# Optimization experiments

Hardware: AMD Instinct MI355X
Metric: run time of the kernel (lower is better)

The kernel has to match this reference:

```python
import jax, jax.numpy as jnp
import numpy as np

N, C, BINS = 4194304, 8, 10


def setup_inputs() -> dict:
    key = jax.random.key(0)
    k1, k2, k3 = jax.random.split(key, 3)
    pred = jax.random.normal(k1, (N, C), dtype=jnp.float32)
    target = jax.random.randint(k2, (N,), 0, C)
    # per-class loss weights (BaseLoss.reset_epoch output), strictly positive
    weight = jax.random.uniform(k3, (C,), dtype=jnp.float32) + 0.5
    return {"pred": pred, "target": target, "weight": weight, "bins": BINS}


def reference(pred, target, weight, bins):
    n_class = pred.shape[1]
    y = jax.nn.one_hot(target, n_class, dtype=pred.dtype)          # [N, C]
    # per-sample class weight broadcast to [N, C] (matches repeat in torch)
    w = jnp.broadcast_to(weight[target][:, None], pred.shape)      # [N, C]

    # gradient norm g = |sigmoid(pred) - y|, detached in the original
    g = jax.lax.stop_gradient(jnp.abs(jax.nn.sigmoid(pred) - y))   # [N, C]
    tot = pred.size

    # edges = arange(bins+1)/bins with edges[-1] += 1e-6, half-open bins:
    # bin index = floor(g * bins), clipped so g == 1.0 lands in the last bin.
    bin_idx = jnp.clip((g * bins).astype(jnp.int32), 0, bins - 1)  # [N, C]

    # single fused histogram pass (replaces the O(bins*N) masked loop)
    counts = jnp.zeros((bins,), pred.dtype).at[bin_idx.ravel()].add(1.0)
    n_nonempty = jnp.sum(counts > 0).astype(pred.dtype)
    per_bin_w = jnp.where(counts > 0, tot / jnp.maximum(counts, 1.0), 0.0)
    ghm_w = per_bin_w[bin_idx] / jnp.maximum(n_nonempty, 1.0)      # [N, C]
    ghm_w = jax.lax.stop_gradient(ghm_w)

    # binary_cross_entropy_with_logits, reduction='none':
    # softplus(x) - x*y  ==  max(x,0) - x*y + log1p(exp(-|x|))
    bce = jax.nn.softplus(pred) - pred * y                         # [N, C]

    return jnp.sum(w * bce * ghm_w) / jnp.sum(w)
```

## Files before the change

### kernel.cpp

```cpp
#include <hip/hip_runtime.h>


#define NROWS 4194304
#define BINS 10

constexpr int BLOCK = 256;
constexpr int MAXGRID = 2048;

__global__ __launch_bounds__(BLOCK) void ghm_main(
    const float* __restrict__ pred, const int* __restrict__ target,
    const float* __restrict__ weight, float* __restrict__ ws)
{
    __shared__ float wlds[8];
    const int tid = threadIdx.x;
    if (tid < 8) wlds[tid] = weight[tid];
    __syncthreads();

    float sP[10];
#pragma unroll
    for (int i = 0; i < 10; ++i) sP[i] = 0.f;
    unsigned cP[10];
#pragma unroll
    for (int i = 0; i < 10; ++i) cP[i] = 0u;
    float sumw = 0.f;

    const int stride = gridDim.x * BLOCK;

    constexpr float NLOG2E = -1.4426950408889634f;
    constexpr float LN2    = 0.6931471805599453f;
    constexpr float A0 = 2.1972245773362196f;
    constexpr float A1 = 1.3862943611198906f;
    constexpr float A2 = 0.8472978603872037f;
    constexpr float A3 = 0.4054651081081644f;
    const unsigned LUT0 = 0x1u, LUT1 = 0x41u, LUT2 = 0x1041u,
                   LUT3 = 0x41041u, LUT4 = 0x1041041u;

    for (int r = blockIdx.x * BLOCK + tid; r < NROWS; ) {
        unsigned aHi = 0u, aLo = 0u;
#pragma unroll
        for (int k = 0; k < 4; ++k, r += stride) {
            const float4 p0 = reinterpret_cast<const float4*>(pred)[2 * r];
            const float4 p1 = reinterpret_cast<const float4*>(pred)[2 * r + 1];
            const int t = target[r];
            const float w = wlds[t];
            sumw += w;
            const float wln2 = w * LN2;
            const float pv[8] = {p0.x, p0.y, p0.z, p0.w, p1.x, p1.y, p1.z, p1.w};
#pragma unroll
            for (int c = 0; c < 8; ++c) {
                const float p = pv[c];
                const float q = (c == t) ? -p : p;
                const float aq = __builtin_fabsf(q);
                const float e = __builtin_amdgcn_exp2f(aq * NLOG2E);
                const bool c0 = aq < A0, c1 = aq < A1, c2 = aq < A2, c3 = aq < A3;
                const bool qp = q >= 0.f;
                const float l = __builtin_amdgcn_logf(1.0f + e);
                const float v = fmaf(l, wln2, w * fmaxf(q, 0.f));
                const float vhi = qp ? v : 0.f;
                const float vlo = v - vhi;
                sP[0] += vhi;               sP[5] += vlo;
                sP[1] += c0 ? vhi : 0.f;    sP[6] += c0 ? vlo : 0.f;
                sP[2] += c1 ? vhi : 0.f;    sP[7] += c1 ? vlo : 0.f;
                sP[3] += c2 ? vhi : 0.f;    sP[8] += c2 ? vlo : 0.f;
                sP[4] += c3 ? vhi : 0.f;    sP[9] += c3 ? vlo : 0.f;
                unsigned lut = c0 ? LUT1 : LUT0;
                lut = c1 ? LUT2 : lut;
                lut = c2 ? LUT3 : lut;
                lut = c3 ? LUT4 : lut;
                const unsigned ih = qp ? lut : 0u;
                aHi += ih;
                aLo += lut - ih;
            }
        }
#pragma unroll
        for (int i = 0; i < 5; ++i) {
            cP[i]     += (aHi >> (6 * i)) & 63u;
            cP[5 + i] += (aLo >> (6 * i)) & 63u;
        }
    }

#pragma unroll
    for (int i = 0; i < 10; ++i) {
        float x = sP[i]; unsigned ci = cP[i];
#pragma unroll
        for (int o = 32; o >= 1; o >>= 1) {
            x  += __shfl_xor(x, o, 64);
            ci += __shfl_xor(ci, o, 64);
        }
        sP[i] = x; cP[i] = ci;
    }
    {
        float x = sumw;
#pragma unroll
        for (int o = 32; o >= 1; o >>= 1) x += __shfl_xor(x, o, 64);
        sumw = x;
    }

    __shared__ float red[4][21];
    const int lane = tid & 63, wv = tid >> 6;
    if (lane == 0) {
#pragma unroll
        for (int i = 0; i < 10; ++i) red[wv][i] = sP[i];
#pragma unroll
        for (int i = 0; i < 10; ++i) red[wv][10 + i] = (float)cP[i];
        red[wv][20] = sumw;
    }
    __syncthreads();
    if (tid < 21) {
        const float s = red[0][tid] + red[1][tid] + red[2][tid] + red[3][tid];
        const int slot = tid < 10 ? tid : (tid < 20 ? tid + 6 : 10);
        ws[blockIdx.x * 32 + slot] = s;
    }
}

__global__ __launch_bounds__(BLOCK) void ghm_final(
    const float* __restrict__ ws, float* __restrict__ out, int nblocks)
{
    float a21[21];
#pragma unroll
    for (int i = 0; i < 21; ++i) a21[i] = 0.f;

    for (int b = threadIdx.x; b < nblocks; b += BLOCK) {
#pragma unroll
        for (int i = 0; i < 10; ++i) a21[i] += ws[b * 32 + i];
#pragma unroll
        for (int i = 0; i < 10; ++i) a21[10 + i] += ws[b * 32 + 16 + i];
        a21[20] += ws[b * 32 + 10];
    }

#pragma unroll
    for (int i = 0; i < 21; ++i) {
        float x = a21[i];
#pragma unroll
        for (int o = 32; o >= 1; o >>= 1) x += __shfl_xor(x, o, 64);
        a21[i] = x;
    }

    __shared__ float red[4][21];
    const int tid = threadIdx.x;
    const int lane = tid & 63, wv = tid >> 6;
    if (lane == 0) {
#pragma unroll
        for (int i = 0; i < 21; ++i) red[wv][i] = a21[i];
    }
    __syncthreads();
    if (tid == 0) {
        float T[21];
#pragma unroll
        for (int i = 0; i < 21; ++i)
            T[i] = red[0][i] + red[1][i] + red[2][i] + red[3][i];
        float S[10], CN[10];
#pragma unroll
        for (int k = 0; k < 5; ++k) {
            const float shn = (k < 4) ? T[k + 1]      : 0.f;
            const float sln = (k < 4) ? T[5 + k + 1]  : 0.f;
            const float chn = (k < 4) ? T[10 + k + 1] : 0.f;
            const float cln = (k < 4) ? T[15 + k + 1] : 0.f;
            S[9 - k]  = T[k]      - shn;  CN[9 - k] = T[10 + k] - chn;
            S[k]      = T[5 + k]  - sln;  CN[k]     = T[15 + k] - cln;
        }
        int nne = 0; float acc = 0.f;
        const float tot = 33554432.0f;
#pragma unroll
        for (int i = 0; i < 10; ++i) {
            if (CN[i] > 0.5f) { nne++; acc += S[i] * (tot / CN[i]); }
        }
        out[0] = acc / (float)nne / (8.0f * T[20]);
    }
}

extern "C" void kernel_launch(void* const* d_in, const int* in_sizes, int n_in,
                              void* d_out, int out_size, void* d_ws, size_t ws_size,
                              hipStream_t stream) {
    const float* pred   = (const float*)d_in[0];
    const int*   target = (const int*)d_in[1];
    const float* weight = (const float*)d_in[2];
    float* out = (float*)d_out;

    int blocks = MAXGRID;
    if (ws_size < (size_t)MAXGRID * 128u) {
        const int cap = (int)(ws_size / 128u);
        blocks = 1;
        while (blocks * 2 <= cap && blocks * 2 < MAXGRID) blocks *= 2;
    }

    ghm_main<<<blocks, BLOCK, 0, stream>>>(pred, target, weight, (float*)d_ws);
    ghm_final<<<1, BLOCK, 0, stream>>>((const float*)d_ws, out, blocks);
}
```

Measured before the change: 56.00 us.

## Specialize main kernel for full grid with all loads issued up front

Adds a specialized kernel for the full 2048-block grid in which each thread handles exactly 8 rows. All target and pred loads are issued before any compute, which raises memory-level parallelism and drops the loop. The per-element math now uses 2-wide float vectors to encourage packed FP32 adds, and the kernel requests 3 blocks per CU via launch bounds. A general grid-stride fallback is kept for small workspaces; the cost is higher register pressure from holding 16 float4 values live at once.

```diff
diff --git a/kernel.cpp b/kernel.cpp
--- a/kernel.cpp
+++ b/kernel.cpp
@@ -5,9 +5,88 @@
 #define BINS 10
 
 constexpr int BLOCK = 256;
-constexpr int MAXGRID = 2048;
-
-__global__ __launch_bounds__(BLOCK) void ghm_main(
+constexpr int GRID  = 2048;
+constexpr int STRD  = GRID * BLOCK;
+
+typedef float f2 __attribute__((ext_vector_type(2)));
+
+__device__ __forceinline__ void elem8(
+    const float4 a, const float4 b, const int t, const float w,
+    f2& sp0, f2& sp1, f2& sp2, f2& sp3, f2& sp4,
+    unsigned& aAll, unsigned& aHi)
+{
+    constexpr float NLOG2E = -1.4426950408889634f;
+    constexpr float LN2    = 0.6931471805599453f;
+    constexpr float T0 = 2.1972245773362196f;
+    constexpr float T1 = 1.3862943611198906f;
+    constexpr float T2 = 0.8472978603872037f;
+    constexpr float T3 = 0.4054651081081644f;
+    const float wln2 = w * LN2;
+    const float pv[8] = {a.x, a.y, a.z, a.w, b.x, b.y, b.z, b.w};
+#pragma unroll
+    for (int c = 0; c < 8; ++c) {
+        const float p = pv[c];
+        const float q = (c == t) ? -p : p;
+        const float aq = __builtin_fabsf(q);
+        const float e = __builtin_amdgcn_exp2f(aq * NLOG2E);
+        const bool b0 = aq < T0, b1 = aq < T1, b2 = aq < T2, b3 = aq < T3;
+        const bool qp = q >= 0.f;
+        const float l = __builtin_amdgcn_logf(1.0f + e);
+        const float v = fmaf(l, wln2, w * fmaxf(q, 0.f));
+        f2 vp; vp.x = qp ? v : 0.f; vp.y = v - vp.x;
+        sp0 += vp;
+        f2 g;
+        g.x = b0 ? vp.x : 0.f; g.y = b0 ? vp.y : 0.f; sp1 += g;
+        g.x = b1 ? vp.x : 0.f; g.y = b1 ? vp.y : 0.f; sp2 += g;
+        g.x = b2 ? vp.x : 0.f; g.y = b2 ? vp.y : 0.f; sp3 += g;
+        g.x = b3 ? vp.x : 0.f; g.y = b3 ? vp.y : 0.f; sp4 += g;
+        unsigned lut = b0 ? 0x41u : 0x1u;
+        lut = b1 ? 0x1041u : lut;
+        lut = b2 ? 0x41041u : lut;
+        lut = b3 ? 0x1041041u : lut;
+        aAll += lut;
+        aHi  += qp ? lut : 0u;
+    }
+}
+
+__device__ __forceinline__ void block_reduce_store(
+    f2 sp0, f2 sp1, f2 sp2, f2 sp3, f2 sp4,
+    const unsigned* cA, const unsigned* cH, float sumw,
+    float* __restrict__ ws, int tid)
+{
+    float r21[21];
+    r21[0] = sp0.x; r21[1] = sp1.x; r21[2] = sp2.x; r21[3] = sp3.x; r21[4] = sp4.x;
+    r21[5] = sp0.y; r21[6] = sp1.y; r21[7] = sp2.y; r21[8] = sp3.y; r21[9] = sp4.y;
+#pragma unroll
+    for (int k = 0; k < 5; ++k) {
+        r21[10 + k] = (float)cH[k];
+        r21[15 + k] = (float)(cA[k] - cH[k]);
+    }
+    r21[20] = sumw;
+
+#pragma unroll
+    for (int i = 0; i < 21; ++i) {
+        float x = r21[i];
+#pragma unroll
+        for (int o = 32; o >= 1; o >>= 1) x += __shfl_xor(x, o, 64);
+        r21[i] = x;
+    }
+
+    __shared__ float red4[4][21];
+    const int lane = tid & 63, wv = tid >> 6;
+    if (lane == 0) {
+#pragma unroll
+        for (int i = 0; i < 21; ++i) red4[wv][i] = r21[i];
+    }
+    __syncthreads();
+    if (tid < 21) {
+        const float s = red4[0][tid] + red4[1][tid] + red4[2][tid] + red4[3][tid];
+        const int slot = tid < 10 ? tid : (tid < 20 ? tid + 6 : 10);
+        ws[blockIdx.x * 32 + slot] = s;
+    }
+}
+
+__global__ __launch_bounds__(BLOCK, 3) void ghm_main_s(
     const float* __restrict__ pred, const int* __restrict__ target,
     const float* __restrict__ weight, float* __restrict__ ws)
 {
@@ -16,101 +95,86 @@
     if (tid < 8) wlds[tid] = weight[tid];
     __syncthreads();
 
-    float sP[10];
-#pragma unroll
-    for (int i = 0; i < 10; ++i) sP[i] = 0.f;
-    unsigned cP[10];
-#pragma unroll
-    for (int i = 0; i < 10; ++i) cP[i] = 0u;
+    const int r0 = blockIdx.x * BLOCK + tid;
+    const float4* __restrict__ p4 = reinterpret_cast<const float4*>(pred);
+
+    int tt[8];
+#pragma unroll
+    for (int i = 0; i < 8; ++i) tt[i] = target[r0 + i * STRD];
+
+    float4 c0a = p4[2 * (size_t)(r0 + 0 * STRD)], c0b = p4[2 * (size_t)(r0 + 0 * STRD) + 1];
+    float4 c1a = p4[2 * (size_t)(r0 + 1 * STRD)], c1b = p4[2 * (size_t)(r0 + 1 * STRD) + 1];
+    float4 c2a = p4[2 * (size_t)(r0 + 2 * STRD)], c2b = p4[2 * (size_t)(r0 + 2 * STRD) + 1];
+    float4 c3a = p4[2 * (size_t)(r0 + 3 * STRD)], c3b = p4[2 * (size_t)(r0 + 3 * STRD) + 1];
+
+    float wr[8];
+#pragma unroll
+    for (int i = 0; i < 8; ++i) wr[i] = wlds[tt[i]];
+
+    float4 n0a = p4[2 * (size_t)(r0 + 4 * STRD)], n0b = p4[2 * (size_t)(r0 + 4 * STRD) + 1];
+    float4 n1a = p4[2 * (size_t)(r0 + 5 * STRD)], n1b = p4[2 * (size_t)(r0 + 5 * STRD) + 1];
+    float4 n2a = p4[2 * (size_t)(r0 + 6 * STRD)], n2b = p4[2 * (size_t)(r0 + 6 * STRD) + 1];
+    float4 n3a = p4[2 * (size_t)(r0 + 7 * STRD)], n3b = p4[2 * (size_t)(r0 + 7 * STRD) + 1];
+
+    f2 sp0 = {0, 0}, sp1 = {0, 0}, sp2 = {0, 0}, sp3 = {0, 0}, sp4 = {0, 0};
+    unsigned cA[5] = {0, 0, 0, 0, 0}, cH[5] = {0, 0, 0, 0, 0};
+    unsigned aAll = 0u, aHi = 0u;
+    const float sumw = ((wr[0] + wr[1]) + (wr[2] + wr[3])) +
+                       ((wr[4] + wr[5]) + (wr[6] + wr[7]));
+
+    elem8(c0a, c0b, tt[0], wr[0], sp0, sp1, sp2, sp3, sp4, aAll, aHi);
+    elem8(c1a, c1b, tt[1], wr[1], sp0, sp1, sp2, sp3, sp4, aAll, aHi);
+    elem8(c2a, c2b, tt[2], wr[2], sp0, sp1, sp2, sp3, sp4, aAll, aHi);
+    elem8(c3a, c3b, tt[3], wr[3], sp0, sp1, sp2, sp3, sp4, aAll, aHi);
+#pragma unroll
+    for (int k = 0; k < 5; ++k) {
+        cA[k] += (aAll >> (6 * k)) & 63u;
+        cH[k] += (aHi  >> (6 * k)) & 63u;
+    }
+    aAll = 0u; aHi = 0u;
+
+    elem8(n0a, n0b, tt[4], wr[4], sp0, sp1, sp2, sp3, sp4, aAll, aHi);
+    elem8(n1a, n1b, tt[5], wr[5], sp0, sp1, sp2, sp3, sp4, aAll, aHi);
+    elem8(n2a, n2b, tt[6], wr[6], sp0, sp1, sp2, sp3, sp4, aAll, aHi);
+    elem8(n3a, n3b, tt[7], wr[7], sp0, sp1, sp2, sp3, sp4, aAll, aHi);
+#pragma unroll
+    for (int k = 0; k < 5; ++k) {
+        cA[k] += (aAll >> (6 * k)) & 63u;
+        cH[k] += (aHi  >> (6 * k)) & 63u;
+    }
+
+    block_reduce_store(sp0, sp1, sp2, sp3, sp4, cA, cH, sumw, ws, tid);
+}
+
+__global__ __launch_bounds__(BLOCK) void ghm_main_d(
+    const float* __restrict__ pred, const int* __restrict__ target,
+    const float* __restrict__ weight, float* __restrict__ ws)
+{
+    __shared__ float wlds[8];
+    const int tid = threadIdx.x;
+    if (tid < 8) wlds[tid] = weight[tid];
+    __syncthreads();
+
+    f2 sp0 = {0, 0}, sp1 = {0, 0}, sp2 = {0, 0}, sp3 = {0, 0}, sp4 = {0, 0};
+    unsigned cA[5] = {0, 0, 0, 0, 0}, cH[5] = {0, 0, 0, 0, 0};
     float sumw = 0.f;
-
     const int stride = gridDim.x * BLOCK;
-
-    constexpr float NLOG2E = -1.4426950408889634f;
-    constexpr float LN2    = 0.6931471805599453f;
-    constexpr float A0 = 2.1972245773362196f;
-    constexpr float A1 = 1.3862943611198906f;
-    constexpr float A2 = 0.8472978603872037f;
-    constexpr float A3 = 0.4054651081081644f;
-    const unsigned LUT0 = 0x1u, LUT1 = 0x41u, LUT2 = 0x1041u,
-                   LUT3 = 0x41041u, LUT4 = 0x1041041u;
-
-    for (int r = blockIdx.x * BLOCK + tid; r < NROWS; ) {
-        unsigned aHi = 0u, aLo = 0u;
-#pragma unroll
-        for (int k = 0; k < 4; ++k, r += stride) {
-            const float4 p0 = reinterpret_cast<const float4*>(pred)[2 * r];
-            const float4 p1 = reinterpret_cast<const float4*>(pred)[2 * r + 1];
-            const int t = target[r];
-            const float w = wlds[t];
-            sumw += w;
-            const float wln2 = w * LN2;
-            const float pv[8] = {p0.x, p0.y, p0.z, p0.w, p1.x, p1.y, p1.z, p1.w};
-#pragma unroll
-            for (int c = 0; c < 8; ++c) {
-                const float p = pv[c];
-                const float q = (c == t) ? -p : p;
-                const float aq = __builtin_fabsf(q);
-                const float e = __builtin_amdgcn_exp2f(aq * NLOG2E);
-                const bool c0 = aq < A0, c1 = aq < A1, c2 = aq < A2, c3 = aq < A3;
-                const bool qp = q >= 0.f;
-                const float l = __builtin_amdgcn_logf(1.0f + e);
-                const float v = fmaf(l, wln2, w * fmaxf(q, 0.f));
-                const float vhi = qp ? v : 0.f;
-                const float vlo = v - vhi;
-                sP[0] += vhi;               sP[5] += vlo;
-                sP[1] += c0 ? vhi : 0.f;    sP[6] += c0 ? vlo : 0.f;
-                sP[2] += c1 ? vhi : 0.f;    sP[7] += c1 ? vlo : 0.f;
-                sP[3] += c2 ? vhi : 0.f;    sP[8] += c2 ? vlo : 0.f;
-                sP[4] += c3 ? vhi : 0.f;    sP[9] += c3 ? vlo : 0.f;
-                unsigned lut = c0 ? LUT1 : LUT0;
-                lut = c1 ? LUT2 : lut;
-                lut = c2 ? LUT3 : lut;
-                lut = c3 ? LUT4 : lut;
-                const unsigned ih = qp ? lut : 0u;
-                aHi += ih;
-                aLo += lut - ih;
-            }
+    const float4* __restrict__ p4 = reinterpret_cast<const float4*>(pred);
+
+    for (int r = blockIdx.x * BLOCK + tid; r < NROWS; r += stride) {
+        const float4 a = p4[2 * (size_t)r], b = p4[2 * (size_t)r + 1];
+        const int t = target[r];
+        const float w = wlds[t];
+        sumw += w;
+        unsigned aAll = 0u, aHi = 0u;
+        elem8(a, b, t, w, sp0, sp1, sp2, sp3, sp4, aAll, aHi);
+#pragma unroll
+        for (int k = 0; k < 5; ++k) {
+            cA[k] += (aAll >> (6 * k)) & 63u;
+            cH[k] += (aHi  >> (6 * k)) & 63u;
         }
-#pragma unroll
-        for (int i = 0; i < 5; ++i) {
-            cP[i]     += (aHi >> (6 * i)) & 63u;
-            cP[5 + i] += (aLo >> (6 * i)) & 63u;
-        }
-    }
-
-#pragma unroll
-    for (int i = 0; i < 10; ++i) {
-        float x = sP[i]; unsigned ci = cP[i];
-#pragma unroll
-        for (int o = 32; o >= 1; o >>= 1) {
-            x  += __shfl_xor(x, o, 64);
-            ci += __shfl_xor(ci, o, 64);
-        }
-        sP[i] = x; cP[i] = ci;
-    }
-    {
-        float x = sumw;
-#pragma unroll
-        for (int o = 32; o >= 1; o >>= 1) x += __shfl_xor(x, o, 64);
-        sumw = x;
-    }
-
-    __shared__ float red[4][21];
-    const int lane = tid & 63, wv = tid >> 6;
-    if (lane == 0) {
-#pragma unroll
-        for (int i = 0; i < 10; ++i) red[wv][i] = sP[i];
-#pragma unroll
-        for (int i = 0; i < 10; ++i) red[wv][10 + i] = (float)cP[i];
-        red[wv][20] = sumw;
-    }
-    __syncthreads();
-    if (tid < 21) {
-        const float s = red[0][tid] + red[1][tid] + red[2][tid] + red[3][tid];
-        const int slot = tid < 10 ? tid : (tid < 20 ? tid + 6 : 10);
-        ws[blockIdx.x * 32 + slot] = s;
-    }
+    }
+    block_reduce_store(sp0, sp1, sp2, sp3, sp4, cA, cH, sumw, ws, tid);
 }
 
 __global__ __launch_bounds__(BLOCK) void ghm_final(
@@ -156,8 +220,8 @@
             const float sln = (k < 4) ? T[5 + k + 1]  : 0.f;
             const float chn = (k < 4) ? T[10 + k + 1] : 0.f;
             const float cln = (k < 4) ? T[15 + k + 1] : 0.f;
-            S[9 - k]  = T[k]      - shn;  CN[9 - k] = T[10 + k] - chn;
-            S[k]      = T[5 + k]  - sln;  CN[k]     = T[15 + k] - cln;
+            S[9 - k] = T[k]     - shn;  CN[9 - k] = T[10 + k] - chn;
+            S[k]     = T[5 + k] - sln;  CN[k]     = T[15 + k] - cln;
         }
         int nne = 0; float acc = 0.f;
         const float tot = 33554432.0f;
@@ -177,13 +241,15 @@
     const float* weight = (const float*)d_in[2];
     float* out = (float*)d_out;
 
-    int blocks = MAXGRID;
-    if (ws_size < (size_t)MAXGRID * 128u) {
+    int blocks;
+    if (ws_size >= (size_t)GRID * 128u) {
+        blocks = GRID;
+        ghm_main_s<<<GRID, BLOCK, 0, stream>>>(pred, target, weight, (float*)d_ws);
+    } else {
         const int cap = (int)(ws_size / 128u);
         blocks = 1;
-        while (blocks * 2 <= cap && blocks * 2 < MAXGRID) blocks *= 2;
-    }
-
-    ghm_main<<<blocks, BLOCK, 0, stream>>>(pred, target, weight, (float*)d_ws);
+        while (blocks * 2 <= cap && blocks * 2 < GRID) blocks *= 2;
+        ghm_main_d<<<blocks, BLOCK, 0, stream>>>(pred, target, weight, (float*)d_ws);
+    }
     ghm_final<<<1, BLOCK, 0, stream>>>((const float*)d_ws, out, blocks);
 }
```

Measured after the change: 92.66 us. 1.65x slower.

## Count histogram bins with wave ballots and use packed float2 accumulators

Applied to the files above, without the earlier changes.

Per-thread packed-LUT bin counting is replaced by wave-wide ballot plus popcount. This moves the count bookkeeping from vector select/add instructions to scalar mask operations, and the counts no longer need a cross-lane shuffle reduction. The ten float partial sums become five float2 vectors, so the compiler can emit packed FP32 adds. The count path assumes all 64 lanes are active on every iteration, which holds only because the row count divides evenly by the grid stride.

```diff
diff --git a/kernel.cpp b/kernel.cpp
--- a/kernel.cpp
+++ b/kernel.cpp
@@ -2,10 +2,91 @@
 
 
 #define NROWS 4194304
-#define BINS 10
 
 constexpr int BLOCK = 256;
 constexpr int MAXGRID = 2048;
+
+typedef float f2 __attribute__((ext_vector_type(2)));
+
+__device__ __forceinline__ void elem8(
+    const float4 a, const float4 b, const int t, const float w,
+    f2& sp0, f2& sp1, f2& sp2, f2& sp3, f2& sp4,
+    unsigned (&cA)[5], unsigned (&cH)[5])
+{
+    constexpr float NLOG2E = -1.4426950408889634f;
+    constexpr float LN2    = 0.6931471805599453f;
+    constexpr float T0 = 2.1972245773362196f;
+    constexpr float T1 = 1.3862943611198906f;
+    constexpr float T2 = 0.8472978603872037f;
+    constexpr float T3 = 0.4054651081081644f;
+    const float wln2 = w * LN2;
+    const float pv[8] = {a.x, a.y, a.z, a.w, b.x, b.y, b.z, b.w};
+#pragma unroll
+    for (int c = 0; c < 8; ++c) {
+        const float p = pv[c];
+        const float q = (c == t) ? -p : p;
+        const float aq = __builtin_fabsf(q);
+        const float e = __builtin_amdgcn_exp2f(aq * NLOG2E);
+        const bool b0 = aq < T0, b1 = aq < T1, b2 = aq < T2, b3 = aq < T3;
+        const bool qp = q >= 0.f;
+        const float l = __builtin_amdgcn_logf(1.0f + e);
+        const float v = fmaf(l, wln2, w * fmaxf(q, 0.f));
+        f2 vp; vp.x = qp ? v : 0.f; vp.y = v - vp.x;
+        sp0 += vp;
+        f2 g;
+        g.x = b0 ? vp.x : 0.f; g.y = b0 ? vp.y : 0.f; sp1 += g;
+        g.x = b1 ? vp.x : 0.f; g.y = b1 ? vp.y : 0.f; sp2 += g;
+        g.x = b2 ? vp.x : 0.f; g.y = b2 ? vp.y : 0.f; sp3 += g;
+        g.x = b3 ? vp.x : 0.f; g.y = b3 ? vp.y : 0.f; sp4 += g;
+        cA[0] += 64u;
+        cH[0] += (unsigned)__popcll(__ballot(qp));
+        cA[1] += (unsigned)__popcll(__ballot(b0));
+        cH[1] += (unsigned)__popcll(__ballot(qp && b0));
+        cA[2] += (unsigned)__popcll(__ballot(b1));
+        cH[2] += (unsigned)__popcll(__ballot(qp && b1));
+        cA[3] += (unsigned)__popcll(__ballot(b2));
+        cH[3] += (unsigned)__popcll(__ballot(qp && b2));
+        cA[4] += (unsigned)__popcll(__ballot(b3));
+        cH[4] += (unsigned)__popcll(__ballot(qp && b3));
+    }
+}
+
+__device__ __forceinline__ void block_reduce_store(
+    f2 sp0, f2 sp1, f2 sp2, f2 sp3, f2 sp4,
+    const unsigned (&cA)[5], const unsigned (&cH)[5], float sumw,
+    float* __restrict__ ws, int tid)
+{
+    float r11[11];
+    r11[0] = sp0.x; r11[1] = sp1.x; r11[2] = sp2.x; r11[3] = sp3.x; r11[4] = sp4.x;
+    r11[5] = sp0.y; r11[6] = sp1.y; r11[7] = sp2.y; r11[8] = sp3.y; r11[9] = sp4.y;
+    r11[10] = sumw;
+
+#pragma unroll
+    for (int i = 0; i < 11; ++i) {
+        float x = r11[i];
+#pragma unroll
+        for (int o = 32; o >= 1; o >>= 1) x += __shfl_xor(x, o, 64);
+        r11[i] = x;
+    }
+
+    __shared__ float red4[4][21];
+    const int lane = tid & 63, wv = tid >> 6;
+    if (lane == 0) {
+#pragma unroll
+        for (int i = 0; i < 11; ++i) red4[wv][i] = r11[i];
+#pragma unroll
+        for (int k = 0; k < 5; ++k) {
+            red4[wv][11 + k] = (float)cH[k];
+            red4[wv][16 + k] = (float)(cA[k] - cH[k]);
+        }
+    }
+    __syncthreads();
+    if (tid < 21) {
+        const float s = red4[0][tid] + red4[1][tid] + red4[2][tid] + red4[3][tid];
+        const int slot = tid < 11 ? tid : tid + 5;
+        ws[blockIdx.x * 32 + slot] = s;
+    }
+}
 
 __global__ __launch_bounds__(BLOCK) void ghm_main(
     const float* __restrict__ pred, const int* __restrict__ target,
@@ -16,101 +97,23 @@
     if (tid < 8) wlds[tid] = weight[tid];
     __syncthreads();
 
-    float sP[10];
-#pragma unroll
-    for (int i = 0; i < 10; ++i) sP[i] = 0.f;
-    unsigned cP[10];
-#pragma unroll
-    for (int i = 0; i < 10; ++i) cP[i] = 0u;
+    f2 sp0 = {0, 0}, sp1 = {0, 0}, sp2 = {0, 0}, sp3 = {0, 0}, sp4 = {0, 0};
+    unsigned cA[5] = {0, 0, 0, 0, 0}, cH[5] = {0, 0, 0, 0, 0};
     float sumw = 0.f;
-
     const int stride = gridDim.x * BLOCK;
-
-    constexpr float NLOG2E = -1.4426950408889634f;
-    constexpr float LN2    = 0.6931471805599453f;
-    constexpr float A0 = 2.1972245773362196f;
-    constexpr float A1 = 1.3862943611198906f;
-    constexpr float A2 = 0.8472978603872037f;
-    constexpr float A3 = 0.4054651081081644f;
-    const unsigned LUT0 = 0x1u, LUT1 = 0x41u, LUT2 = 0x1041u,
-                   LUT3 = 0x41041u, LUT4 = 0x1041041u;
+    const float4* __restrict__ p4 = reinterpret_cast<const float4*>(pred);
 
     for (int r = blockIdx.x * BLOCK + tid; r < NROWS; ) {
-        unsigned aHi = 0u, aLo = 0u;
 #pragma unroll
         for (int k = 0; k < 4; ++k, r += stride) {
-            const float4 p0 = reinterpret_cast<const float4*>(pred)[2 * r];
-            const float4 p1 = reinterpret_cast<const float4*>(pred)[2 * r + 1];
+            const float4 a = p4[2 * (size_t)r], b = p4[2 * (size_t)r + 1];
             const int t = target[r];
             const float w = wlds[t];
             sumw += w;
-            const float wln2 = w * LN2;
-            const float pv[8] = {p0.x, p0.y, p0.z, p0.w, p1.x, p1.y, p1.z, p1.w};
-#pragma unroll
-            for (int c = 0; c < 8; ++c) {
-                const float p = pv[c];
-                const float q = (c == t) ? -p : p;
-                const float aq = __builtin_fabsf(q);
-                const float e = __builtin_amdgcn_exp2f(aq * NLOG2E);
-                const bool c0 = aq < A0, c1 = aq < A1, c2 = aq < A2, c3 = aq < A3;
-                const bool qp = q >= 0.f;
-                const float l = __builtin_amdgcn_logf(1.0f + e);
-                const float v = fmaf(l, wln2, w * fmaxf(q, 0.f));
-                const float vhi = qp ? v : 0.f;
-                const float vlo = v - vhi;
-                sP[0] += vhi;               sP[5] += vlo;
-                sP[1] += c0 ? vhi : 0.f;    sP[6] += c0 ? vlo : 0.f;
-                sP[2] += c1 ? vhi : 0.f;    sP[7] += c1 ? vlo : 0.f;
-                sP[3] += c2 ? vhi : 0.f;    sP[8] += c2 ? vlo : 0.f;
-                sP[4] += c3 ? vhi : 0.f;    sP[9] += c3 ? vlo : 0.f;
-                unsigned lut = c0 ? LUT1 : LUT0;
-                lut = c1 ? LUT2 : lut;
-                lut = c2 ? LUT3 : lut;
-                lut = c3 ? LUT4 : lut;
-                const unsigned ih = qp ? lut : 0u;
-                aHi += ih;
-                aLo += lut - ih;
-            }
-        }
-#pragma unroll
-        for (int i = 0; i < 5; ++i) {
-            cP[i]     += (aHi >> (6 * i)) & 63u;
-            cP[5 + i] += (aLo >> (6 * i)) & 63u;
+            elem8(a, b, t, w, sp0, sp1, sp2, sp3, sp4, cA, cH);
         }
     }
-
-#pragma unroll
-    for (int i = 0; i < 10; ++i) {
-        float x = sP[i]; unsigned ci = cP[i];
-#pragma unroll
-        for (int o = 32; o >= 1; o >>= 1) {
-            x  += __shfl_xor(x, o, 64);
-            ci += __shfl_xor(ci, o, 64);
-        }
-        sP[i] = x; cP[i] = ci;
-    }
-    {
-        float x = sumw;
-#pragma unroll
-        for (int o = 32; o >= 1; o >>= 1) x += __shfl_xor(x, o, 64);
-        sumw = x;
-    }
-
-    __shared__ float red[4][21];
-    const int lane = tid & 63, wv = tid >> 6;
-    if (lane == 0) {
-#pragma unroll
-        for (int i = 0; i < 10; ++i) red[wv][i] = sP[i];
-#pragma unroll
-        for (int i = 0; i < 10; ++i) red[wv][10 + i] = (float)cP[i];
-        red[wv][20] = sumw;
-    }
-    __syncthreads();
-    if (tid < 21) {
-        const float s = red[0][tid] + red[1][tid] + red[2][tid] + red[3][tid];
-        const int slot = tid < 10 ? tid : (tid < 20 ? tid + 6 : 10);
-        ws[blockIdx.x * 32 + slot] = s;
-    }
+    block_reduce_store(sp0, sp1, sp2, sp3, sp4, cA, cH, sumw, ws, tid);
 }
 
 __global__ __launch_bounds__(BLOCK) void ghm_final(
@@ -156,8 +159,8 @@
             const float sln = (k < 4) ? T[5 + k + 1]  : 0.f;
             const float chn = (k < 4) ? T[10 + k + 1] : 0.f;
             const float cln = (k < 4) ? T[15 + k + 1] : 0.f;
-            S[9 - k]  = T[k]      - shn;  CN[9 - k] = T[10 + k] - chn;
-            S[k]      = T[5 + k]  - sln;  CN[k]     = T[15 + k] - cln;
+            S[9 - k] = T[k]     - shn;  CN[9 - k] = T[10 + k] - chn;
+            S[k]     = T[5 + k] - sln;  CN[k]     = T[15 + k] - cln;
         }
         int nne = 0; float acc = 0.f;
         const float tot = 33554432.0f;
```

Measured after the change: 54.47 us. 2.7% less time.
